# Kernel tuning notes

Hardware: AMD Instinct MI355X
Metric: run time of the kernel (lower is better)

## Reference

```python
import jax, jax.numpy as jnp
import numpy as np

N = 20000      # num_nodes / scatter_size
F = 128        # dataset_num_features
H = 8          # heads
HID = 64       # hidden_channels
REP = 512      # represent_features
NCLS = 133     # dataset_num_classes
E = 200000     # num edges (== num synapses)
PTS = 4        # points per synapse
P = E * PTS    # total synapse points

# Eval-mode semantics: dropout = identity; PyG MLP BatchNorm with fresh
# running stats (mean=0, var=1, affine=1/0) = identity. GATConv has no
# edge_dim, so edge_attr does not enter the math (kept as an input for parity).

def _glorot(key, shape):
    fan_in, fan_out = shape[0], shape[-1]
    if len(shape) == 3:  # attention vectors [H, C]: PyG treats as (1, H*C)
        fan_in, fan_out = 1, shape[-2] * shape[-1]
    lim = jnp.sqrt(6.0 / (fan_in + fan_out))
    return jax.random.uniform(key, shape, jnp.float32, -lim, lim)


def setup_inputs() -> dict:
    key = jax.random.key(0)
    ks = jax.random.split(key, 20)
    edge_index = jax.random.randint(ks[0], (2, E), 0, N, dtype=jnp.int32)
    edge_attr = jax.random.normal(ks[1], (E, 1), jnp.float32)
    synapse = jax.random.normal(ks[2], (P, 6), jnp.float32)
    # every synapse (edge) owns PTS points -> no empty segments for max-pool
    synapse_index = (jnp.arange(P, dtype=jnp.int32) // PTS)
    inp = {
        "edge_index": edge_index,
        "edge_attr": edge_attr,
        "synapse": synapse,
        "synapse_index": synapse_index,
        "scatter_size": N,
        # learned node embedding (nn.Parameter, xavier)
        "x_param": _glorot(ks[3], (N, F)),
        # GATConv 1: F -> H*HID
        "W1": _glorot(ks[4], (F, H * HID)),
        "att_src1": _glorot(ks[5], (1, H, HID))[0],
        "att_dst1": _glorot(ks[6], (1, H, HID))[0],
        "b1": jnp.zeros((H * HID,), jnp.float32),
        # GATConv 2: H*HID -> REP, heads=1, concat=False
        "W2": _glorot(ks[7], (H * HID, REP)),
        "att_src2": _glorot(ks[8], (1, 1, REP))[0],
        "att_dst2": _glorot(ks[9], (1, 1, REP))[0],
        "b2": jnp.zeros((REP,), jnp.float32),
        # synapse_encoder MLP([6, 256, 512])
        "We1": _glorot(ks[10], (6, 256)),
        "be1": jnp.zeros((256,), jnp.float32),
        "We2": _glorot(ks[11], (256, 512)),
        "be2": jnp.zeros((512,), jnp.float32),
        # classmodel MLP([1536, 512, 133])
        "Wc1": _glorot(ks[12], (1536, 512)),
        "bc1": jnp.zeros((512,), jnp.float32),
        "Wc2": _glorot(ks[13], (512, NCLS)),
        "bc2": jnp.zeros((NCLS,), jnp.float32),
    }
    return inp


def _gat_conv(x, src, dst, n, W, a_src, a_dst, b, heads, ch, concat):
    # x: [n, Fin]; src/dst already include self-loops (PyG default)
    xl = (x @ W).reshape(n, heads, ch)                 # [n, H, C]
    s = jnp.einsum('nhc,hc->nh', xl, a_src)            # alpha_src
    d = jnp.einsum('nhc,hc->nh', xl, a_dst)            # alpha_dst
    alpha = jax.nn.leaky_relu(s[src] + d[dst], negative_slope=0.2)  # [Ee, H]
    amax = jax.ops.segment_max(alpha, dst, num_segments=n)
    ex = jnp.exp(alpha - amax[dst])
    den = jax.ops.segment_sum(ex, dst, num_segments=n)
    a = ex / (den[dst] + 1e-16)                        # segment softmax
    out = jax.ops.segment_sum(xl[src] * a[:, :, None], dst, num_segments=n)
    out = out.reshape(n, heads * ch) if concat else out.mean(axis=1)
    return out + b


def _scatter_mean(vals, idx, n):
    s = jax.ops.segment_sum(vals, idx, num_segments=n)
    cnt = jax.ops.segment_sum(jnp.ones((vals.shape[0],), vals.dtype), idx, num_segments=n)
    return s / jnp.maximum(cnt, 1.0)[:, None]


def reference(edge_index, edge_attr, synapse, synapse_index, scatter_size,
              x_param, W1, att_src1, att_dst1, b1, W2, att_src2, att_dst2, b2,
              We1, be1, We2, be2, Wc1, bc1, Wc2, bc2):
    n = scatter_size
    loop = jnp.arange(n, dtype=edge_index.dtype)
    src = jnp.concatenate([edge_index[0], loop])   # GATConv adds self-loops
    dst = jnp.concatenate([edge_index[1], loop])

    x = jax.nn.elu(_gat_conv(x_param, src, dst, n, W1, att_src1, att_dst1, b1, H, HID, True))
    x = _gat_conv(x, src, dst, n, W2, att_src2, att_dst2, b2, 1, REP, False)   # [n, REP]

    # global_max_pool over synapse points -> one 6-vec per edge
    x_point = jax.ops.segment_max(synapse, synapse_index, num_segments=E)      # [E, 6]
    x_point = jax.nn.relu(x_point @ We1 + be1) @ We2 + be2                      # [E, 512]

    left = _scatter_mean(x_point, edge_index[0], n)
    right = _scatter_mean(x_point, edge_index[1], n)

    final = jnp.concatenate([x, left, right], axis=1)                           # [n, 1536]
    pred = jax.nn.relu(final @ Wc1 + bc1) @ Wc2 + bc2
    return pred
```

## Files before the change

kernel.cpp:

```cpp
#include <hip/hip_runtime.h>
#include <cstddef>

#define NN   20000
#define FEAT 128
#define NH   8
#define NE   200000
#define EE   220000

typedef _Float16 f16;
typedef _Float16 f16x2 __attribute__((ext_vector_type(2)));
typedef _Float16 f16x8 __attribute__((ext_vector_type(8)));
typedef float    f32x4 __attribute__((ext_vector_type(4)));

__device__ __forceinline__ float lrelu(float a) { return a > 0.f ? a : 0.2f * a; }

#define PB0 782
#define PB1 (PB0 + 782)
#define PB2 (PB1 + 10064)
#define PB3 (PB2 + 10)
#define PB4 (PB3 + 128)
#define PB5 (PB4 + 80)
__global__ __launch_bounds__(256) void preamble(
    const int* __restrict__ ei, const float* __restrict__ syn,
    const float* __restrict__ W1, const float* __restrict__ xparam,
    const float* __restrict__ W2, const float* __restrict__ We2,
    const float* __restrict__ Wc1, const float* __restrict__ Wc2,
    const float* __restrict__ b2, const float* __restrict__ be2,
    const float* __restrict__ as2, const float* __restrict__ ad2,
    int* __restrict__ dL, int* __restrict__ dR,
    float* __restrict__ xp, f16* __restrict__ W1t, f16* __restrict__ xph,
    f16* __restrict__ WzAt, f16* __restrict__ McatT, f16* __restrict__ Wc2t,
    float* __restrict__ vB, float* __restrict__ vL, float* __restrict__ vR,
    float* __restrict__ ws2, float* __restrict__ wd2)
{
  __shared__ float smem[2112];
  const int b = blockIdx.x, t = threadIdx.x;
  if (b < PB0) {
    int e = b * 256 + t;
    if (e >= NE) return;
    atomicAdd(&dL[ei[e]], 1);
    atomicAdd(&dR[ei[NE + e]], 1);
  } else if (b < PB1) {
    int e = (b - PB0) * 256 + t;
    if (e >= NE) return;
    const float* p = syn + (size_t)e * 24;
    float v[24];
#pragma unroll
    for (int i = 0; i < 6; i++) {
      float4 q = *(const float4*)(p + i * 4);
      v[i*4+0] = q.x; v[i*4+1] = q.y; v[i*4+2] = q.z; v[i*4+3] = q.w;
    }
#pragma unroll
    for (int dd = 0; dd < 6; dd++)
      xp[(size_t)e * 6 + dd] = fmaxf(fmaxf(v[dd], v[6 + dd]), fmaxf(v[12 + dd], v[18 + dd]));
  } else if (b < PB2) {
    int bb = b - PB1;
    if (bb < 64) {
      float (*tile)[33] = (float(*)[33])smem;
      const int n0 = (bb & 15) * 32, k0 = (bb >> 4) * 32;
      const int tx = t & 31, ty = t >> 5;
#pragma unroll
      for (int i = 0; i < 4; i++)
        tile[ty + i * 8][tx] = W1[(size_t)(k0 + ty + i * 8) * 512 + n0 + tx];
      __syncthreads();
#pragma unroll
      for (int i = 0; i < 4; i++)
        W1t[(size_t)(n0 + ty + i * 8) * 128 + k0 + tx] = (f16)tile[tx][ty + i * 8];
    } else {
      int idx = (bb - 64) * 256 + t;
      xph[idx] = (f16)xparam[idx];
    }
  } else if (b < PB3) {
    int g = (b - PB2) * 256 + t;
    int seg = g >> 9, j = g & 511;
    float a = 0.f;
    if (seg == 0) {
      for (int k = 0; k < 512; k++) a = fmaf(b2[k], Wc1[(size_t)k * 512 + j], a);
      vB[j] = a;
    } else if (seg == 1) {
      for (int k = 0; k < 512; k++) a = fmaf(be2[k], Wc1[(size_t)(512 + k) * 512 + j], a);
      vL[j] = a;
    } else if (seg == 2) {
      for (int k = 0; k < 512; k++) a = fmaf(be2[k], Wc1[(size_t)(1024 + k) * 512 + j], a);
      vR[j] = a;
    } else if (seg == 3) {
      for (int c = 0; c < 512; c++) a = fmaf(W2[(size_t)j * 512 + c], as2[c], a);
      ws2[j] = a;
    } else {
      for (int c = 0; c < 512; c++) a = fmaf(W2[(size_t)j * 512 + c], ad2[c], a);
      wd2[j] = a;
    }
  } else if (b < PB4) {
    float (*As)[68] = (float(*)[68])smem;
    float (*Bs)[64] = (float(*)[64])(smem + 16 * 68);
    const int bb = b - PB3;
    const float* A; const float* B; f16* dst; int dstOff, m0, n0;
    if (bb < 64)      { A = W2;  B = Wc1;  dst = WzAt;  dstOff = 0;
                        m0 = (bb >> 3) * 64; n0 = (bb & 7) * 64; }
    else if (bb < 96) { int i = bb - 64; A = We2; B = Wc1 + (size_t)512 * 512;
                        dst = McatT; dstOff = 0;
                        m0 = (i >> 3) * 64; n0 = (i & 7) * 64; }
    else              { int i = bb - 96; A = We2; B = Wc1 + (size_t)1024 * 512;
                        dst = McatT; dstOff = 256;
                        m0 = (i >> 3) * 64; n0 = (i & 7) * 64; }
    const int tx = t & 15, ty = t >> 4;
    float acc[4][4] = {{0.f}};
    float pa[4], pb[4];
#pragma unroll
    for (int i = 0; i < 4; i++) {
      int idx = t + i * 256;
      pa[i] = A[(size_t)(m0 + (idx >> 4)) * 512 + (idx & 15)];
      pb[i] = B[(size_t)(idx >> 6) * 512 + n0 + (idx & 63)];
    }
    for (int k0 = 0; k0 < 512; k0 += 16) {
#pragma unroll
      for (int i = 0; i < 4; i++) {
        int idx = t + i * 256;
        As[idx & 15][idx >> 4] = pa[i];
        Bs[idx >> 6][idx & 63] = pb[i];
      }
      __syncthreads();
      if (k0 + 16 < 512) {
        int kn = k0 + 16;
#pragma unroll
        for (int i = 0; i < 4; i++) {
          int idx = t + i * 256;
          pa[i] = A[(size_t)(m0 + (idx >> 4)) * 512 + kn + (idx & 15)];
          pb[i] = B[(size_t)(kn + (idx >> 6)) * 512 + n0 + (idx & 63)];
        }
      }
#pragma unroll
      for (int kk = 0; kk < 16; kk++) {
        float4 a4 = *(const float4*)&As[kk][ty * 4];
        float4 b4 = *(const float4*)&Bs[kk][tx * 4];
        float av[4] = {a4.x, a4.y, a4.z, a4.w};
        float bv[4] = {b4.x, b4.y, b4.z, b4.w};
#pragma unroll
        for (int i = 0; i < 4; i++)
#pragma unroll
          for (int j = 0; j < 4; j++) acc[i][j] = fmaf(av[i], bv[j], acc[i][j]);
      }
      __syncthreads();
    }
#pragma unroll
    for (int i = 0; i < 4; i++)
#pragma unroll
      for (int j = 0; j < 4; j++)
        dst[(size_t)(n0 + tx * 4 + j) * 512 + dstOff + m0 + ty * 4 + i] = (f16)acc[i][j];
  } else {
    float (*tile)[33] = (float(*)[33])smem;
    int i0 = b - PB4;
    const int n0 = (i0 % 5) * 32, k0 = (i0 / 5) * 32;
    const int tx = t & 31, ty = t >> 5;
#pragma unroll
    for (int i = 0; i < 4; i++) {
      int k = k0 + ty + i * 8, n = n0 + tx;
      tile[ty + i * 8][tx] = (n < 133) ? Wc2[(size_t)k * 133 + n] : 0.f;
    }
    __syncthreads();
#pragma unroll
    for (int i = 0; i < 4; i++) {
      int n = n0 + ty + i * 8, k = k0 + tx;
      if (n < 133) Wc2t[(size_t)n * 512 + k] = (f16)tile[tx][ty + i * 8];
    }
  }
}

__global__ __launch_bounds__(256) void fused1(
    const f16* __restrict__ xph, const f16* __restrict__ W1t, f16* __restrict__ xl1h,
    const float* __restrict__ xp, const float* __restrict__ We1,
    const float* __restrict__ be1,
    const int* __restrict__ oL, const int* __restrict__ eL,
    const int* __restrict__ oR, const int* __restrict__ eR,
    f16* __restrict__ hlrh)
{
  __shared__ __align__(16) f16 smem[7680];
  const int t = threadIdx.x;
  if (blockIdx.x < 1252) {
    f16 (*As)[40] = (f16(*)[40])smem;
    f16 (*Bs)[40] = (f16(*)[40])(smem + 64 * 40);
    const int wave = t >> 6, lane = t & 63;
    const int quad = lane >> 4, mrow = lane & 15;
    const int m0 = (blockIdx.x >> 2) * 64, n0 = (blockIdx.x & 3) * 128;
    f32x4 acc[4][2];
    f32x4 zero4 = {0.f, 0.f, 0.f, 0.f};
#pragma unroll
    for (int i = 0; i < 4; i++)
#pragma unroll
      for (int j = 0; j < 2; j++) acc[i][j] = zero4;
    const int ar = t >> 2, ac = (t & 3) * 8;
    for (int k0 = 0; k0 < FEAT; k0 += 32) {
      {
        int gm = m0 + ar;
        f16x8 v = {0, 0, 0, 0, 0, 0, 0, 0};
        if (gm < NN) v = *(const f16x8*)(xph + (size_t)gm * FEAT + k0 + ac);
        *(f16x8*)&As[ar][ac] = v;
      }
#pragma unroll
      for (int i = 0; i < 2; i++) {
        int idx = t + i * 256;
        int r = idx >> 2, c = (idx & 3) * 8;
        *(f16x8*)&Bs[r][c] = *(const f16x8*)(W1t + (size_t)(n0 + r) * FEAT + k0 + c);
      }
      __syncthreads();
      f16x8 af[4], bf[2];
#pragma unroll
      for (int mt = 0; mt < 4; mt++) af[mt] = *(const f16x8*)&As[mt * 16 + mrow][quad * 8];
#pragma unroll
      for (int nt = 0; nt < 2; nt++) bf[nt] = *(const f16x8*)&Bs[wave * 32 + nt * 16 + mrow][quad * 8];
#pragma unroll
      for (int mt = 0; mt < 4; mt++)
#pragma unroll
        for (int nt = 0; nt < 2; nt++)
          acc[mt][nt] = __builtin_amdgcn_mfma_f32_16x16x32_f16(af[mt], bf[nt], acc[mt][nt], 0, 0, 0);
      __syncthreads();
    }
#pragma unroll
    for (int mt = 0; mt < 4; mt++)
#pragma unroll
      for (int nt = 0; nt < 2; nt++) {
        int col = n0 + wave * 32 + nt * 16 + mrow;
#pragma unroll
        for (int reg = 0; reg < 4; reg++) {
          int row = m0 + mt * 16 + quad * 4 + reg;
          if (row < NN) xl1h[(size_t)row * 512 + col] = (f16)acc[mt][nt][reg];
        }
      }
  } else {
    int* lst_s  = (int*)smem;
    f16x2* xs2  = (f16x2*)(smem + 128);
    const int b = blockIdx.x - 1252;
    const int c = t;
    const int* off; const int* lst; int n;
    if (b < NN) { off = oL; lst = eL; n = b; } else { off = oR; lst = eR; n = b - NN; }
    f16x2 w[6], bb2, zero2;
#pragma unroll
    for (int j = 0; j < 6; j++) { f16 wv = (f16)We1[j * 256 + c]; w[j][0] = wv; w[j][1] = wv; }
    { f16 bv = (f16)be1[c]; bb2[0] = bv; bb2[1] = bv; }
    zero2[0] = (f16)0.f; zero2[1] = (f16)0.f;
    const int beg = off[n], end = off[n + 1], deg = end - beg;
    f16x2 acc2 = zero2;
    float accT = 0.f;
    for (int base = 0; base < deg; base += 32) {
      int m = min(32, deg - base);
      if (c < 32) lst_s[c] = (c < m) ? lst[beg + base + c] : 0;
      __syncthreads();
      if (c < 96) {
        int j = c / 6, cc = c - j * 6;
        int e0 = 2 * j, e1 = 2 * j + 1;
        float v0 = (e0 < m) ? xp[(size_t)lst_s[e0] * 6 + cc] : 0.f;
        float v1 = (e1 < m) ? xp[(size_t)lst_s[e1] * 6 + cc] : 0.f;
        f16x2 pr; pr[0] = (f16)v0; pr[1] = (f16)v1;
        xs2[j * 6 + cc] = pr;
      }
      __syncthreads();
      int mp = m >> 1;
      for (int k = 0; k < mp; k++) {
        f16x2 v = bb2;
#pragma unroll
        for (int j = 0; j < 6; j++) v = xs2[k * 6 + j] * w[j] + v;
        f16x2 r;
        r[0] = v[0] > (f16)0.f ? v[0] : (f16)0.f;
        r[1] = v[1] > (f16)0.f ? v[1] : (f16)0.f;
        acc2 = acc2 + r;
      }
      if (m & 1) {
        float v = (float)bb2[0];
#pragma unroll
        for (int j = 0; j < 6; j++) v = fmaf((float)xs2[mp * 6 + j][0], (float)w[j][0], v);
        accT += fmaxf(v, 0.f);
      }
    }
    float accf = (float)acc2[0] + (float)acc2[1] + accT;
    hlrh[(size_t)b * 256 + c] = (f16)(deg > 0 ? accf / (float)deg : 0.f);
  }
}

__global__ __launch_bounds__(256) void fused2(
    const f16* __restrict__ x1h, const f16* __restrict__ WzAt, f16* __restrict__ zh,
    const f16* __restrict__ hlrh, const f16* __restrict__ McatT,
    const int* __restrict__ degL, const int* __restrict__ degR,
    const float* __restrict__ bc1, const float* __restrict__ vB,
    const float* __restrict__ vL, const float* __restrict__ vR, f16* __restrict__ Ph)
{
  __shared__ __align__(16) f16 smem[7680];
  const int t = threadIdx.x;
  f16 (*As)[40] = (f16(*)[40])smem;
  f16 (*Bs)[40] = (f16(*)[40])(smem + 64 * 40);
  const bool isZ = blockIdx.x < 1252;
  const int bb = isZ ? blockIdx.x : blockIdx.x - 1252;
  const int wave = t >> 6, lane = t & 63;
  const int quad = lane >> 4, mrow = lane & 15;
  const int m0 = (bb >> 2) * 64, n0 = (bb & 3) * 128;
  f32x4 acc[4][2];
  f32x4 zero4 = {0.f, 0.f, 0.f, 0.f};
#pragma unroll
  for (int i = 0; i < 4; i++)
#pragma unroll
    for (int j = 0; j < 2; j++) acc[i][j] = zero4;
  const int ar = t >> 2, ac = (t & 3) * 8;
  const f16* Bt = isZ ? WzAt : McatT;
  for (int k0 = 0; k0 < 512; k0 += 32) {
    {
      int gm = m0 + ar;
      f16x8 v = {0, 0, 0, 0, 0, 0, 0, 0};
      if (gm < NN) {
        if (isZ) v = *(const f16x8*)(x1h + (size_t)gm * 512 + k0 + ac);
        else {
          size_t row = (k0 >> 8) ? (size_t)(NN + gm) : (size_t)gm;
          v = *(const f16x8*)(hlrh + row * 256 + (k0 & 255) + ac);
        }
      }
      *(f16x8*)&As[ar][ac] = v;
    }
#pragma unroll
    for (int i = 0; i < 2; i++) {
      int idx = t + i * 256;
      int r = idx >> 2, c = (idx & 3) * 8;
      *(f16x8*)&Bs[r][c] = *(const f16x8*)(Bt + (size_t)(n0 + r) * 512 + k0 + c);
    }
    __syncthreads();
    f16x8 af[4], bf[2];
#pragma unroll
    for (int mt = 0; mt < 4; mt++) af[mt] = *(const f16x8*)&As[mt * 16 + mrow][quad * 8];
#pragma unroll
    for (int nt = 0; nt < 2; nt++) bf[nt] = *(const f16x8*)&Bs[wave * 32 + nt * 16 + mrow][quad * 8];
#pragma unroll
    for (int mt = 0; mt < 4; mt++)
#pragma unroll
      for (int nt = 0; nt < 2; nt++)
        acc[mt][nt] = __builtin_amdgcn_mfma_f32_16x16x32_f16(af[mt], bf[nt], acc[mt][nt], 0, 0, 0);
    __syncthreads();
  }
  if (isZ) {
#pragma unroll
    for (int mt = 0; mt < 4; mt++)
#pragma unroll
      for (int nt = 0; nt < 2; nt++) {
        int col = n0 + wave * 32 + nt * 16 + mrow;
#pragma unroll
        for (int reg = 0; reg < 4; reg++) {
          int row = m0 + mt * 16 + quad * 4 + reg;
          if (row < NN) zh[(size_t)row * 512 + col] = (f16)acc[mt][nt][reg];
        }
      }
  } else {
#pragma unroll
    for (int mt = 0; mt < 4; mt++)
#pragma unroll
      for (int nt = 0; nt < 2; nt++) {
        int col = n0 + wave * 32 + nt * 16 + mrow;
        float bb2 = bc1[col] + vB[col];
        float vl = vL[col], vr = vR[col];
#pragma unroll
        for (int reg = 0; reg < 4; reg++) {
          int row = m0 + mt * 16 + quad * 4 + reg;
          if (row >= NN) continue;
          float v = acc[mt][nt][reg] + bb2;
          if (degL[row] > 0) v += vl;
          if (degR[row] > 0) v += vr;
          Ph[(size_t)row * 512 + col] = (f16)v;
        }
      }
  }
}

__global__ __launch_bounds__(256) void mfma_out(
    const f16* __restrict__ A, const f16* __restrict__ Bt,
    const float* __restrict__ bias, float* __restrict__ C, int M)
{
  __shared__ __align__(16) f16 As[64][40];
  __shared__ __align__(16) f16 Bs[128][40];
  const int t = threadIdx.x;
  const int wave = t >> 6, lane = t & 63;
  const int quad = lane >> 4, mrow = lane & 15;
  const int m0 = blockIdx.y * 64, n0 = blockIdx.x * 128;
  f32x4 acc[4][2];
  f32x4 zero4 = {0.f, 0.f, 0.f, 0.f};
#pragma unroll
  for (int i = 0; i < 4; i++)
#pragma unroll
    for (int j = 0; j < 2; j++) acc[i][j] = zero4;
  const int ar = t >> 2, ac = (t & 3) * 8;
  for (int k0 = 0; k0 < 512; k0 += 32) {
    {
      int gm = m0 + ar;
      f16x8 v = {0, 0, 0, 0, 0, 0, 0, 0};
      if (gm < M) v = *(const f16x8*)(A + (size_t)gm * 512 + k0 + ac);
      *(f16x8*)&As[ar][ac] = v;
    }
#pragma unroll
    for (int i = 0; i < 2; i++) {
      int idx = t + i * 256;
      int r = idx >> 2, c = (idx & 3) * 8;
      f16x8 v = {0, 0, 0, 0, 0, 0, 0, 0};
      if (n0 + r < 133) v = *(const f16x8*)(Bt + (size_t)(n0 + r) * 512 + k0 + c);
      *(f16x8*)&Bs[r][c] = v;
    }
    __syncthreads();
    f16x8 af[4], bf[2];
#pragma unroll
    for (int mt = 0; mt < 4; mt++) af[mt] = *(const f16x8*)&As[mt * 16 + mrow][quad * 8];
#pragma unroll
    for (int nt = 0; nt < 2; nt++) bf[nt] = *(const f16x8*)&Bs[wave * 32 + nt * 16 + mrow][quad * 8];
#pragma unroll
    for (int mt = 0; mt < 4; mt++)
#pragma unroll
      for (int nt = 0; nt < 2; nt++)
        acc[mt][nt] = __builtin_amdgcn_mfma_f32_16x16x32_f16(af[mt], bf[nt], acc[mt][nt], 0, 0, 0);
    __syncthreads();
  }
#pragma unroll
  for (int mt = 0; mt < 4; mt++)
#pragma unroll
    for (int nt = 0; nt < 2; nt++) {
      int col = n0 + wave * 32 + nt * 16 + mrow;
      if (col >= 133) continue;
      float bb = bias[col];
#pragma unroll
      for (int reg = 0; reg < 4; reg++) {
        int row = m0 + mt * 16 + quad * 4 + reg;
        if (row < M) C[(size_t)row * 133 + col] = acc[mt][nt][reg] + bb;
      }
    }
}

__global__ __launch_bounds__(1024) void scan_csr(
    const int* __restrict__ dL, const int* __restrict__ dR,
    int* __restrict__ oL, int* __restrict__ oR, int* __restrict__ oA)
{
  const int b = blockIdx.x;
  const int* deg = b == 0 ? dL : dR;
  __shared__ int part[1024];
  const int t = threadIdx.x;
  const int chunk = 20;
  int base = t * chunk;
  int sum = 0;
  for (int i = 0; i < chunk; i++) { int idx = base + i; if (idx < NN) sum += deg[idx]; }
  part[t] = sum;
  __syncthreads();
  for (int o = 1; o < 1024; o <<= 1) {
    int v = (t >= o) ? part[t - o] : 0;
    __syncthreads();
    part[t] += v;
    __syncthreads();
  }
  int run = part[t] - sum;
  if (b == 0) {
    for (int i = 0; i < chunk; i++) {
      int idx = base + i;
      if (idx < NN) { oL[idx] = run; run += deg[idx]; }
    }
    if (t == 0) oL[NN] = part[1023];
  } else {
    for (int i = 0; i < chunk; i++) {
      int idx = base + i;
      if (idx < NN) { oR[idx] = run; oA[idx] = run + idx; run += deg[idx]; }
    }
    if (t == 0) { oR[NN] = part[1023]; oA[NN] = part[1023] + NN; }
  }
}

__global__ __launch_bounds__(256) void fill_csr(
    const int* __restrict__ ei,
    const int* __restrict__ oL, const int* __restrict__ oR, const int* __restrict__ oA,
    int* __restrict__ cL, int* __restrict__ cR,
    int* __restrict__ eL, int* __restrict__ eR, int* __restrict__ snA)
{
  int e = blockIdx.x * 256 + threadIdx.x;
  if (e >= EE) return;
  if (e < NE) {
    int s = ei[e], d = ei[NE + e];
    int p = atomicAdd(&cL[s], 1); eL[oL[s] + p] = e;
    p = atomicAdd(&cR[d], 1);
    eR[oR[d] + p] = e;
    snA[oA[d] + 1 + p] = s;
  } else {
    int n = e - NE;
    snA[oA[n]] = n;
  }
}

__global__ __launch_bounds__(256) void attn_dots1(
    const f16* __restrict__ xlh, const float* __restrict__ asrc,
    const float* __restrict__ adst, float* __restrict__ s, float* __restrict__ d)
{
  int gid = blockIdx.x * 256 + threadIdx.x;
  if (gid >= NN * NH) return;
  int n = gid >> 3, h = gid & 7;
  const f16x2* row = (const f16x2*)(xlh + (size_t)n * 512 + h * 64);
  const float* a1 = asrc + h * 64;
  const float* a2 = adst + h * 64;
  float ss = 0.f, dd = 0.f;
#pragma unroll 8
  for (int j = 0; j < 32; j++) {
    f16x2 p = row[j];
    float v0 = (float)p[0], v1 = (float)p[1];
    ss += v0 * a1[2 * j] + v1 * a1[2 * j + 1];
    dd += v0 * a2[2 * j] + v1 * a2[2 * j + 1];
  }
  s[gid] = ss; d[gid] = dd;
}

__global__ __launch_bounds__(256) void gat_gather1(
    const int* __restrict__ snA, const int* __restrict__ offA,
    const float* __restrict__ s1, const float* __restrict__ d1,
    const f16* __restrict__ xlh, const float* __restrict__ b1,
    const float* __restrict__ ws2, const float* __restrict__ wd2,
    f16* __restrict__ x1h, float* __restrict__ s2, float* __restrict__ d2)
{
  __shared__ int sns[32];
  __shared__ float wls[256];
  __shared__ float red[256], redD[256];
  const int n = blockIdx.x, t = threadIdx.x;
  const int hw = t & 7;
  const int slot = t >> 3;
  const int hf = t >> 5;
  const int beg = offA[n], end = offA[n + 1];
  const int deg = end - beg;
  const float dnw = d1[n * 8 + hw];
  float a0 = 0.f, a1v = 0.f, denp = 0.f;
  for (int base = 0; base < deg; base += 32) {
    int m = min(32, deg - base);
    if (t < 32) sns[t] = (t < m) ? snA[beg + base + t] : 0;
    __syncthreads();
    {
      float w = 0.f;
      if (slot < m) w = __expf(lrelu(s1[sns[slot] * 8 + hw] + dnw));
      wls[t] = w;
      denp += w;
    }
    __syncthreads();
    int m8 = (m + 7) & ~7;
    for (int k = 0; k < m8; k += 8) {
      int ss[8]; float ww[8]; f16x2 pp[8];
#pragma unroll
      for (int u = 0; u < 8; u++) { ss[u] = sns[k + u]; ww[u] = wls[(k + u) * 8 + hf]; }
#pragma unroll
      for (int u = 0; u < 8; u++) pp[u] = *(const f16x2*)(xlh + (size_t)ss[u] * 512 + 2 * t);
#pragma unroll
      for (int u = 0; u < 8; u++) {
        a0  = fmaf(ww[u], (float)pp[u][0], a0);
        a1v = fmaf(ww[u], (float)pp[u][1], a1v);
      }
    }
    __syncthreads();
  }
  red[t] = denp;
  __syncthreads();
  for (int off = 128; off >= 8; off >>= 1) {
    if (t < off) red[t] += red[t + off];
    __syncthreads();
  }
  float rh = 1.f / (red[hf] + 1e-16f);
  __syncthreads();
  float v0 = a0 * rh + b1[2 * t], v1 = a1v * rh + b1[2 * t + 1];
  v0 = v0 > 0.f ? v0 : (__expf(v0) - 1.f);
  v1 = v1 > 0.f ? v1 : (__expf(v1) - 1.f);
  f16x2 o; o[0] = (f16)v0; o[1] = (f16)v1;
  *(f16x2*)(x1h + (size_t)n * 512 + 2 * t) = o;
  red[t]  = v0 * ws2[2 * t] + v1 * ws2[2 * t + 1];
  redD[t] = v0 * wd2[2 * t] + v1 * wd2[2 * t + 1];
  __syncthreads();
  for (int off = 128; off > 0; off >>= 1) {
    if (t < off) { red[t] += red[t + off]; redD[t] += redD[t + off]; }
    __syncthreads();
  }
  if (t == 0) { s2[n] = red[0]; d2[n] = redD[0]; }
}

__global__ __launch_bounds__(256) void gat_gather2(
    const int* __restrict__ snA, const int* __restrict__ offA,
    const float* __restrict__ s2, const float* __restrict__ d2,
    const f16* __restrict__ zh, const f16* __restrict__ Ph,
    f16* __restrict__ h2h)
{
  __shared__ int sns[32];
  __shared__ float wls[32];
  __shared__ float den_sh;
  const int n = blockIdx.x, t = threadIdx.x;
  const int beg = offA[n], end = offA[n + 1];
  const int deg = end - beg;
  const float dn = d2[n];
  float a0 = 0.f, a1v = 0.f, denp = 0.f;
  for (int base = 0; base < deg; base += 32) {
    int m = min(32, deg - base);
    if (t < 32) {
      int sn = (t < m) ? snA[beg + base + t] : 0;
      float w = (t < m) ? __expf(lrelu(s2[sn] + dn)) : 0.f;
      sns[t] = sn;
      wls[t] = w;
      denp += w;
    }
    __syncthreads();
    int m8 = (m + 7) & ~7;
    for (int k = 0; k < m8; k += 8) {
      int ss[8]; float ww[8]; f16x2 pp[8];
#pragma unroll
      for (int u = 0; u < 8; u++) { ss[u] = sns[k + u]; ww[u] = wls[k + u]; }
#pragma unroll
      for (int u = 0; u < 8; u++) pp[u] = *(const f16x2*)(zh + (size_t)ss[u] * 512 + 2 * t);
#pragma unroll
      for (int u = 0; u < 8; u++) {
        a0  = fmaf(ww[u], (float)pp[u][0], a0);
        a1v = fmaf(ww[u], (float)pp[u][1], a1v);
      }
    }
    __syncthreads();
  }
  if (t < 64) {
    denp += __shfl_xor(denp, 16);
    denp += __shfl_xor(denp, 8);
    denp += __shfl_xor(denp, 4);
    denp += __shfl_xor(denp, 2);
    denp += __shfl_xor(denp, 1);
    if (t == 0) den_sh = denp;
  }
  __syncthreads();
  float rn = 1.f / (den_sh + 1e-16f);
  f16x2 pv = *(const f16x2*)(Ph + (size_t)n * 512 + 2 * t);
  float v0 = fmaxf(a0  * rn + (float)pv[0], 0.f);
  float v1 = fmaxf(a1v * rn + (float)pv[1], 0.f);
  f16x2 o; o[0] = (f16)v0; o[1] = (f16)v1;
  *(f16x2*)(h2h + (size_t)n * 512 + 2 * t) = o;
}

extern "C" void kernel_launch(void* const* d_in, const int* in_sizes, int n_in,
                              void* d_out, int out_size, void* d_ws, size_t ws_size,
                              hipStream_t stream) {
  const int*   edge_index = (const int*)d_in[0];
  const float* synapse    = (const float*)d_in[2];
  const float* x_param = (const float*)d_in[5];
  const float* W1      = (const float*)d_in[6];
  const float* as1     = (const float*)d_in[7];
  const float* ad1     = (const float*)d_in[8];
  const float* b1      = (const float*)d_in[9];
  const float* W2      = (const float*)d_in[10];
  const float* as2     = (const float*)d_in[11];
  const float* ad2     = (const float*)d_in[12];
  const float* b2      = (const float*)d_in[13];
  const float* We1     = (const float*)d_in[14];
  const float* be1     = (const float*)d_in[15];
  const float* We2     = (const float*)d_in[16];
  const float* be2     = (const float*)d_in[17];
  const float* Wc1     = (const float*)d_in[18];
  const float* bc1     = (const float*)d_in[19];
  const float* Wc2     = (const float*)d_in[20];
  const float* bc2     = (const float*)d_in[21];
  float* out_p = (float*)d_out;

  char* p = (char*)d_ws;
  float* xp    = (float*)p; p += (size_t)NE * 6 * 4;
  float* s1    = (float*)p; p += (size_t)NN * 8 * 4;
  float* d1    = (float*)p; p += (size_t)NN * 8 * 4;
  float* s2    = (float*)p; p += (size_t)NN * 4;
  float* d2    = (float*)p; p += (size_t)NN * 4;
  float* vB    = (float*)p; p += 512 * 4;
  float* vL    = (float*)p; p += 512 * 4;
  float* vR    = (float*)p; p += 512 * 4;
  float* ws2   = (float*)p; p += 512 * 4;
  float* wd2   = (float*)p; p += 512 * 4;
  f16* xph     = (f16*)p; p += (size_t)NN * FEAT * 2;
  f16* xl1h    = (f16*)p; p += (size_t)NN * 512 * 2;
  f16* x1h     = (f16*)p; p += (size_t)NN * 512 * 2;
  f16* zh      = (f16*)p; p += (size_t)NN * 512 * 2;
  f16* h2h     = (f16*)p; p += (size_t)NN * 512 * 2;
  f16* Phb     = (f16*)p; p += (size_t)NN * 512 * 2;
  f16* hlrh    = (f16*)p; p += (size_t)2 * NN * 256 * 2;
  f16* W1t     = (f16*)p; p += (size_t)512 * FEAT * 2;
  f16* WzAt    = (f16*)p; p += (size_t)512 * 512 * 2;
  f16* McatT   = (f16*)p; p += (size_t)512 * 512 * 2;
  f16* Wc2t    = (f16*)p; p += (size_t)133 * 512 * 2;
  int* degL    = (int*)p;
  int* degR    = degL + NN;
  int* curL    = degR + NN;
  int* curR    = curL + NN;
  int* offL    = curR + NN;
  int* offR    = offL + NN + 1;
  int* offA    = offR + NN + 1;
  int* edgeL   = offA + NN + 1;
  int* edgeR   = edgeL + NE;
  int* snA     = edgeR + NE;

  hipMemsetAsync(degL, 0, (size_t)4 * NN * sizeof(int), stream);

  preamble<<<PB5, 256, 0, stream>>>(
      edge_index, synapse, W1, x_param, W2, We2, Wc1, Wc2, b2, be2, as2, ad2,
      degL, degR, xp, W1t, xph, WzAt, McatT, Wc2t, vB, vL, vR, ws2, wd2);
  scan_csr<<<2, 1024, 0, stream>>>(degL, degR, offL, offR, offA);
  fill_csr<<<(EE + 255) / 256, 256, 0, stream>>>(edge_index, offL, offR, offA,
                                                 curL, curR, edgeL, edgeR, snA);
  fused1<<<1252 + 2 * NN, 256, 0, stream>>>(xph, W1t, xl1h, xp, We1, be1,
                                            offL, edgeL, offR, edgeR, hlrh);
  attn_dots1<<<(NN * NH + 255) / 256, 256, 0, stream>>>(xl1h, as1, ad1, s1, d1);
  gat_gather1<<<NN, 256, 0, stream>>>(snA, offA, s1, d1, xl1h, b1, ws2, wd2,
                                      x1h, s2, d2);
  fused2<<<2504, 256, 0, stream>>>(x1h, WzAt, zh, hlrh, McatT,
                                   degL, degR, bc1, vB, vL, vR, Phb);
  gat_gather2<<<NN, 256, 0, stream>>>(snA, offA, s2, d2, zh, Phb, h2h);
  mfma_out<<<dim3(2, 313), 256, 0, stream>>>(h2h, Wc2t, bc2, out_p, NN);
}
```

Before: 489.4 us.

## Fuse attention dots into GEMM epilogue and rebalance weight prep across kernels

The layer-1 attention dot products are now computed in the fused1 GEMM epilogue from an LDS tile, which removes the separate attn_dots1 kernel and its re-read of xl1h. Each edge-pooling block now handles 16 nodes instead of one, cutting the block count from 40000 to 2500. The weight-product GEMMs and the Wc2 transpose move out of the preamble into a new mid_kernel, where they run as extra blocks beside the gather1 work, shortening the critical path through the preamble. The costs are heavier per-block serialization in the pooling path and an extra LDS tile write in the GEMM epilogue.

```diff
diff --git a/kernel.cpp b/kernel.cpp
--- a/kernel.cpp
+++ b/kernel.cpp
@@ -14,34 +14,30 @@
 
 __device__ __forceinline__ float lrelu(float a) { return a > 0.f ? a : 0.2f * a; }
 
-#define PB0 782
-#define PB1 (PB0 + 782)
-#define PB2 (PB1 + 10064)
-#define PB3 (PB2 + 10)
-#define PB4 (PB3 + 128)
-#define PB5 (PB4 + 80)
-__global__ __launch_bounds__(256) void preamble(
+#define PA0 782
+#define PA1 (PA0 + 782)
+#define PA2 (PA1 + 10064)
+#define PA3 (PA2 + 10)
+__global__ __launch_bounds__(256) void preambleA(
     const int* __restrict__ ei, const float* __restrict__ syn,
     const float* __restrict__ W1, const float* __restrict__ xparam,
-    const float* __restrict__ W2, const float* __restrict__ We2,
-    const float* __restrict__ Wc1, const float* __restrict__ Wc2,
+    const float* __restrict__ W2, const float* __restrict__ Wc1,
     const float* __restrict__ b2, const float* __restrict__ be2,
     const float* __restrict__ as2, const float* __restrict__ ad2,
     int* __restrict__ dL, int* __restrict__ dR,
     float* __restrict__ xp, f16* __restrict__ W1t, f16* __restrict__ xph,
-    f16* __restrict__ WzAt, f16* __restrict__ McatT, f16* __restrict__ Wc2t,
     float* __restrict__ vB, float* __restrict__ vL, float* __restrict__ vR,
     float* __restrict__ ws2, float* __restrict__ wd2)
 {
-  __shared__ float smem[2112];
+  __shared__ float smem[1056];
   const int b = blockIdx.x, t = threadIdx.x;
-  if (b < PB0) {
+  if (b < PA0) {
     int e = b * 256 + t;
     if (e >= NE) return;
     atomicAdd(&dL[ei[e]], 1);
     atomicAdd(&dR[ei[NE + e]], 1);
-  } else if (b < PB1) {
-    int e = (b - PB0) * 256 + t;
+  } else if (b < PA1) {
+    int e = (b - PA0) * 256 + t;
     if (e >= NE) return;
     const float* p = syn + (size_t)e * 24;
     float v[24];
@@ -53,8 +49,8 @@
 #pragma unroll
     for (int dd = 0; dd < 6; dd++)
       xp[(size_t)e * 6 + dd] = fmaxf(fmaxf(v[dd], v[6 + dd]), fmaxf(v[12 + dd], v[18 + dd]));
-  } else if (b < PB2) {
-    int bb = b - PB1;
+  } else if (b < PA2) {
+    int bb = b - PA1;
     if (bb < 64) {
       float (*tile)[33] = (float(*)[33])smem;
       const int n0 = (bb & 15) * 32, k0 = (bb >> 4) * 32;
@@ -70,8 +66,8 @@
       int idx = (bb - 64) * 256 + t;
       xph[idx] = (f16)xparam[idx];
     }
-  } else if (b < PB3) {
-    int g = (b - PB2) * 256 + t;
+  } else {
+    int g = (b - PA2) * 256 + t;
     int seg = g >> 9, j = g & 511;
     float a = 0.f;
     if (seg == 0) {
@@ -90,10 +86,226 @@
       for (int c = 0; c < 512; c++) a = fmaf(W2[(size_t)j * 512 + c], ad2[c], a);
       wd2[j] = a;
     }
-  } else if (b < PB4) {
+  }
+}
+
+__global__ __launch_bounds__(256) void fused1(
+    const f16* __restrict__ xph, const f16* __restrict__ W1t, f16* __restrict__ xl1h,
+    const float* __restrict__ as1, const float* __restrict__ ad1,
+    float* __restrict__ s1, float* __restrict__ d1,
+    const float* __restrict__ xp, const float* __restrict__ We1,
+    const float* __restrict__ be1,
+    const int* __restrict__ oL, const int* __restrict__ eL,
+    const int* __restrict__ oR, const int* __restrict__ eR,
+    f16* __restrict__ hlrh)
+{
+  __shared__ __align__(16) f16 smem[8320];
+  const int t = threadIdx.x;
+  if (blockIdx.x < 1252) {
+    f16 (*As)[40] = (f16(*)[40])smem;
+    f16 (*Bs)[40] = (f16(*)[40])(smem + 64 * 40);
+    const int wave = t >> 6, lane = t & 63;
+    const int quad = lane >> 4, mrow = lane & 15;
+    const int m0 = (blockIdx.x >> 2) * 64, n0 = (blockIdx.x & 3) * 128;
+    f32x4 acc[4][2];
+    f32x4 zero4 = {0.f, 0.f, 0.f, 0.f};
+#pragma unroll
+    for (int i = 0; i < 4; i++)
+#pragma unroll
+      for (int j = 0; j < 2; j++) acc[i][j] = zero4;
+    const int ar = t >> 2, ac = (t & 3) * 8;
+    for (int k0 = 0; k0 < FEAT; k0 += 32) {
+      {
+        int gm = m0 + ar;
+        f16x8 v = {0, 0, 0, 0, 0, 0, 0, 0};
+        if (gm < NN) v = *(const f16x8*)(xph + (size_t)gm * FEAT + k0 + ac);
+        *(f16x8*)&As[ar][ac] = v;
+      }
+#pragma unroll
+      for (int i = 0; i < 2; i++) {
+        int idx = t + i * 256;
+        int r = idx >> 2, c = (idx & 3) * 8;
+        *(f16x8*)&Bs[r][c] = *(const f16x8*)(W1t + (size_t)(n0 + r) * FEAT + k0 + c);
+      }
+      __syncthreads();
+      f16x8 af[4], bf[2];
+#pragma unroll
+      for (int mt = 0; mt < 4; mt++) af[mt] = *(const f16x8*)&As[mt * 16 + mrow][quad * 8];
+#pragma unroll
+      for (int nt = 0; nt < 2; nt++) bf[nt] = *(const f16x8*)&Bs[wave * 32 + nt * 16 + mrow][quad * 8];
+#pragma unroll
+      for (int mt = 0; mt < 4; mt++)
+#pragma unroll
+        for (int nt = 0; nt < 2; nt++)
+          acc[mt][nt] = __builtin_amdgcn_mfma_f32_16x16x32_f16(af[mt], bf[nt], acc[mt][nt], 0, 0, 0);
+      __syncthreads();
+    }
+    f16 (*tile)[130] = (f16(*)[130])smem;
+#pragma unroll
+    for (int mt = 0; mt < 4; mt++)
+#pragma unroll
+      for (int nt = 0; nt < 2; nt++) {
+        int cl = wave * 32 + nt * 16 + mrow;
+        int col = n0 + cl;
+#pragma unroll
+        for (int reg = 0; reg < 4; reg++) {
+          int rl = mt * 16 + quad * 4 + reg;
+          int row = m0 + rl;
+          f16 cv = (f16)acc[mt][nt][reg];
+          tile[rl][cl] = cv;
+          if (row < NN) xl1h[(size_t)row * 512 + col] = cv;
+        }
+      }
+    __syncthreads();
+    {
+      int pair = t >> 1, half = t & 1;
+      int rl = pair & 63, hl = pair >> 6;
+      int h = (n0 >> 6) + hl;
+      const float* a1 = as1 + h * 64 + half * 32;
+      const float* a2 = ad1 + h * 64 + half * 32;
+      const f16* trow = &tile[rl][hl * 64 + half * 32];
+      float ssum = 0.f, dsum = 0.f;
+#pragma unroll 8
+      for (int j = 0; j < 32; j++) {
+        float v = (float)trow[j];
+        ssum += v * a1[j];
+        dsum += v * a2[j];
+      }
+      ssum += __shfl_down(ssum, 1);
+      dsum += __shfl_down(dsum, 1);
+      int row = m0 + rl;
+      if (!half && row < NN) { s1[row * 8 + h] = ssum; d1[row * 8 + h] = dsum; }
+    }
+  } else {
+    int* lst_s  = (int*)smem;
+    f16x2* xs2  = (f16x2*)(smem + 128);
+    const int c = t;
+    f16x2 w[6], bb2, zero2;
+#pragma unroll
+    for (int j = 0; j < 6; j++) { f16 wv = (f16)We1[j * 256 + c]; w[j][0] = wv; w[j][1] = wv; }
+    { f16 bv = (f16)be1[c]; bb2[0] = bv; bb2[1] = bv; }
+    zero2[0] = (f16)0.f; zero2[1] = (f16)0.f;
+    const int b0 = (blockIdx.x - 1252) * 16;
+    for (int q = 0; q < 16; q++) {
+      const int b = b0 + q;
+      const int* off; const int* lst; int n;
+      if (b < NN) { off = oL; lst = eL; n = b; } else { off = oR; lst = eR; n = b - NN; }
+      const int beg = off[n], end = off[n + 1], deg = end - beg;
+      f16x2 acc2 = zero2;
+      float accT = 0.f;
+      for (int base = 0; base < deg; base += 32) {
+        int m = min(32, deg - base);
+        if (c < 32) lst_s[c] = (c < m) ? lst[beg + base + c] : 0;
+        __syncthreads();
+        if (c < 96) {
+          int j = c / 6, cc = c - j * 6;
+          int e0 = 2 * j, e1 = 2 * j + 1;
+          float v0 = (e0 < m) ? xp[(size_t)lst_s[e0] * 6 + cc] : 0.f;
+          float v1 = (e1 < m) ? xp[(size_t)lst_s[e1] * 6 + cc] : 0.f;
+          f16x2 pr; pr[0] = (f16)v0; pr[1] = (f16)v1;
+          xs2[j * 6 + cc] = pr;
+        }
+        __syncthreads();
+        int mp = m >> 1;
+        for (int k = 0; k < mp; k++) {
+          f16x2 v = bb2;
+#pragma unroll
+          for (int j = 0; j < 6; j++) v = xs2[k * 6 + j] * w[j] + v;
+          f16x2 r;
+          r[0] = v[0] > (f16)0.f ? v[0] : (f16)0.f;
+          r[1] = v[1] > (f16)0.f ? v[1] : (f16)0.f;
+          acc2 = acc2 + r;
+        }
+        if (m & 1) {
+          float v = (float)bb2[0];
+#pragma unroll
+          for (int j = 0; j < 6; j++) v = fmaf((float)xs2[mp * 6 + j][0], (float)w[j][0], v);
+          accT += fmaxf(v, 0.f);
+        }
+        __syncthreads();
+      }
+      float accf = (float)acc2[0] + (float)acc2[1] + accT;
+      hlrh[(size_t)b * 256 + c] = (f16)(deg > 0 ? accf / (float)deg : 0.f);
+    }
+  }
+}
+
+__global__ __launch_bounds__(256) void mid_kernel(
+    const int* __restrict__ snA, const int* __restrict__ offA,
+    const float* __restrict__ s1, const float* __restrict__ d1,
+    const f16* __restrict__ xlh, const float* __restrict__ b1,
+    const float* __restrict__ ws2, const float* __restrict__ wd2,
+    f16* __restrict__ x1h, float* __restrict__ s2, float* __restrict__ d2,
+    const float* __restrict__ W2, const float* __restrict__ We2,
+    const float* __restrict__ Wc1, f16* __restrict__ WzAt, f16* __restrict__ McatT,
+    const float* __restrict__ Wc2, f16* __restrict__ Wc2t)
+{
+  __shared__ float smem[2112];
+  const int t = threadIdx.x;
+  if (blockIdx.x < NN) {
+    int* sns   = (int*)smem;
+    float* wls = smem + 32;
+    float* red = smem + 288;
+    float* redD= smem + 544;
+    const int n = blockIdx.x;
+    const int hw = t & 7;
+    const int slot = t >> 3;
+    const int hf = t >> 5;
+    const int beg = offA[n], end = offA[n + 1];
+    const int deg = end - beg;
+    const float dnw = d1[n * 8 + hw];
+    float a0 = 0.f, a1v = 0.f, denp = 0.f;
+    for (int base = 0; base < deg; base += 32) {
+      int m = min(32, deg - base);
+      if (t < 32) sns[t] = (t < m) ? snA[beg + base + t] : 0;
+      __syncthreads();
+      {
+        float w = 0.f;
+        if (slot < m) w = __expf(lrelu(s1[sns[slot] * 8 + hw] + dnw));
+        wls[t] = w;
+        denp += w;
+      }
+      __syncthreads();
+      int m8 = (m + 7) & ~7;
+      for (int k = 0; k < m8; k += 8) {
+        int ss[8]; float ww[8]; f16x2 pp[8];
+#pragma unroll
+        for (int u = 0; u < 8; u++) { ss[u] = sns[k + u]; ww[u] = wls[(k + u) * 8 + hf]; }
+#pragma unroll
+        for (int u = 0; u < 8; u++) pp[u] = *(const f16x2*)(xlh + (size_t)ss[u] * 512 + 2 * t);
+#pragma unroll
+        for (int u = 0; u < 8; u++) {
+          a0  = fmaf(ww[u], (float)pp[u][0], a0);
+          a1v = fmaf(ww[u], (float)pp[u][1], a1v);
+        }
+      }
+      __syncthreads();
+    }
+    red[t] = denp;
+    __syncthreads();
+    for (int off = 128; off >= 8; off >>= 1) {
+      if (t < off) red[t] += red[t + off];
+      __syncthreads();
+    }
+    float rh = 1.f / (red[hf] + 1e-16f);
+    __syncthreads();
+    float v0 = a0 * rh + b1[2 * t], v1 = a1v * rh + b1[2 * t + 1];
+    v0 = v0 > 0.f ? v0 : (__expf(v0) - 1.f);
+    v1 = v1 > 0.f ? v1 : (__expf(v1) - 1.f);
+    f16x2 o; o[0] = (f16)v0; o[1] = (f16)v1;
+    *(f16x2*)(x1h + (size_t)n * 512 + 2 * t) = o;
+    red[t]  = v0 * ws2[2 * t] + v1 * ws2[2 * t + 1];
+    redD[t] = v0 * wd2[2 * t] + v1 * wd2[2 * t + 1];
+    __syncthreads();
+    for (int off = 128; off > 0; off >>= 1) {
+      if (t < off) { red[t] += red[t + off]; redD[t] += redD[t + off]; }
+      __syncthreads();
+    }
+    if (t == 0) { s2[n] = red[0]; d2[n] = redD[0]; }
+  } else if (blockIdx.x < NN + 128) {
     float (*As)[68] = (float(*)[68])smem;
     float (*Bs)[64] = (float(*)[64])(smem + 16 * 68);
-    const int bb = b - PB3;
+    const int bb = blockIdx.x - NN;
     const float* A; const float* B; f16* dst; int dstOff, m0, n0;
     if (bb < 64)      { A = W2;  B = Wc1;  dst = WzAt;  dstOff = 0;
                         m0 = (bb >> 3) * 64; n0 = (bb & 7) * 64; }
@@ -149,7 +361,7 @@
         dst[(size_t)(n0 + tx * 4 + j) * 512 + dstOff + m0 + ty * 4 + i] = (f16)acc[i][j];
   } else {
     float (*tile)[33] = (float(*)[33])smem;
-    int i0 = b - PB4;
+    int i0 = blockIdx.x - NN - 128;
     const int n0 = (i0 % 5) * 32, k0 = (i0 / 5) * 32;
     const int tx = t & 31, ty = t >> 5;
 #pragma unroll
@@ -163,116 +375,6 @@
       int n = n0 + ty + i * 8, k = k0 + tx;
       if (n < 133) Wc2t[(size_t)n * 512 + k] = (f16)tile[tx][ty + i * 8];
     }
-  }
-}
-
-__global__ __launch_bounds__(256) void fused1(
-    const f16* __restrict__ xph, const f16* __restrict__ W1t, f16* __restrict__ xl1h,
-    const float* __restrict__ xp, const float* __restrict__ We1,
-    const float* __restrict__ be1,
-    const int* __restrict__ oL, const int* __restrict__ eL,
-    const int* __restrict__ oR, const int* __restrict__ eR,
-    f16* __restrict__ hlrh)
-{
-  __shared__ __align__(16) f16 smem[7680];
-  const int t = threadIdx.x;
-  if (blockIdx.x < 1252) {
-    f16 (*As)[40] = (f16(*)[40])smem;
-    f16 (*Bs)[40] = (f16(*)[40])(smem + 64 * 40);
-    const int wave = t >> 6, lane = t & 63;
-    const int quad = lane >> 4, mrow = lane & 15;
-    const int m0 = (blockIdx.x >> 2) * 64, n0 = (blockIdx.x & 3) * 128;
-    f32x4 acc[4][2];
-    f32x4 zero4 = {0.f, 0.f, 0.f, 0.f};
-#pragma unroll
-    for (int i = 0; i < 4; i++)
-#pragma unroll
-      for (int j = 0; j < 2; j++) acc[i][j] = zero4;
-    const int ar = t >> 2, ac = (t & 3) * 8;
-    for (int k0 = 0; k0 < FEAT; k0 += 32) {
-      {
-        int gm = m0 + ar;
-        f16x8 v = {0, 0, 0, 0, 0, 0, 0, 0};
-        if (gm < NN) v = *(const f16x8*)(xph + (size_t)gm * FEAT + k0 + ac);
-        *(f16x8*)&As[ar][ac] = v;
-      }
-#pragma unroll
-      for (int i = 0; i < 2; i++) {
-        int idx = t + i * 256;
-        int r = idx >> 2, c = (idx & 3) * 8;
-        *(f16x8*)&Bs[r][c] = *(const f16x8*)(W1t + (size_t)(n0 + r) * FEAT + k0 + c);
-      }
-      __syncthreads();
-      f16x8 af[4], bf[2];
-#pragma unroll
-      for (int mt = 0; mt < 4; mt++) af[mt] = *(const f16x8*)&As[mt * 16 + mrow][quad * 8];
-#pragma unroll
-      for (int nt = 0; nt < 2; nt++) bf[nt] = *(const f16x8*)&Bs[wave * 32 + nt * 16 + mrow][quad * 8];
-#pragma unroll
-      for (int mt = 0; mt < 4; mt++)
-#pragma unroll
-        for (int nt = 0; nt < 2; nt++)
-          acc[mt][nt] = __builtin_amdgcn_mfma_f32_16x16x32_f16(af[mt], bf[nt], acc[mt][nt], 0, 0, 0);
-      __syncthreads();
-    }
-#pragma unroll
-    for (int mt = 0; mt < 4; mt++)
-#pragma unroll
-      for (int nt = 0; nt < 2; nt++) {
-        int col = n0 + wave * 32 + nt * 16 + mrow;
-#pragma unroll
-        for (int reg = 0; reg < 4; reg++) {
-          int row = m0 + mt * 16 + quad * 4 + reg;
-          if (row < NN) xl1h[(size_t)row * 512 + col] = (f16)acc[mt][nt][reg];
-        }
-      }
-  } else {
-    int* lst_s  = (int*)smem;
-    f16x2* xs2  = (f16x2*)(smem + 128);
-    const int b = blockIdx.x - 1252;
-    const int c = t;
-    const int* off; const int* lst; int n;
-    if (b < NN) { off = oL; lst = eL; n = b; } else { off = oR; lst = eR; n = b - NN; }
-    f16x2 w[6], bb2, zero2;
-#pragma unroll
-    for (int j = 0; j < 6; j++) { f16 wv = (f16)We1[j * 256 + c]; w[j][0] = wv; w[j][1] = wv; }
-    { f16 bv = (f16)be1[c]; bb2[0] = bv; bb2[1] = bv; }
-    zero2[0] = (f16)0.f; zero2[1] = (f16)0.f;
-    const int beg = off[n], end = off[n + 1], deg = end - beg;
-    f16x2 acc2 = zero2;
-    float accT = 0.f;
-    for (int base = 0; base < deg; base += 32) {
-      int m = min(32, deg - base);
-      if (c < 32) lst_s[c] = (c < m) ? lst[beg + base + c] : 0;
-      __syncthreads();
-      if (c < 96) {
-        int j = c / 6, cc = c - j * 6;
-        int e0 = 2 * j, e1 = 2 * j + 1;
-        float v0 = (e0 < m) ? xp[(size_t)lst_s[e0] * 6 + cc] : 0.f;
-        float v1 = (e1 < m) ? xp[(size_t)lst_s[e1] * 6 + cc] : 0.f;
-        f16x2 pr; pr[0] = (f16)v0; pr[1] = (f16)v1;
-        xs2[j * 6 + cc] = pr;
-      }
-      __syncthreads();
-      int mp = m >> 1;
-      for (int k = 0; k < mp; k++) {
-        f16x2 v = bb2;
-#pragma unroll
-        for (int j = 0; j < 6; j++) v = xs2[k * 6 + j] * w[j] + v;
-        f16x2 r;
-        r[0] = v[0] > (f16)0.f ? v[0] : (f16)0.f;
-        r[1] = v[1] > (f16)0.f ? v[1] : (f16)0.f;
-        acc2 = acc2 + r;
-      }
-      if (m & 1) {
-        float v = (float)bb2[0];
-#pragma unroll
-        for (int j = 0; j < 6; j++) v = fmaf((float)xs2[mp * 6 + j][0], (float)w[j][0], v);
-        accT += fmaxf(v, 0.f);
-      }
-    }
-    float accf = (float)acc2[0] + (float)acc2[1] + accT;
-    hlrh[(size_t)b * 256 + c] = (f16)(deg > 0 ? accf / (float)deg : 0.f);
   }
 }
 
@@ -479,94 +581,6 @@
     int n = e - NE;
     snA[oA[n]] = n;
   }
-}
-
-__global__ __launch_bounds__(256) void attn_dots1(
-    const f16* __restrict__ xlh, const float* __restrict__ asrc,
-    const float* __restrict__ adst, float* __restrict__ s, float* __restrict__ d)
-{
-  int gid = blockIdx.x * 256 + threadIdx.x;
-  if (gid >= NN * NH) return;
-  int n = gid >> 3, h = gid & 7;
-  const f16x2* row = (const f16x2*)(xlh + (size_t)n * 512 + h * 64);
-  const float* a1 = asrc + h * 64;
-  const float* a2 = adst + h * 64;
-  float ss = 0.f, dd = 0.f;
-#pragma unroll 8
-  for (int j = 0; j < 32; j++) {
-    f16x2 p = row[j];
-    float v0 = (float)p[0], v1 = (float)p[1];
-    ss += v0 * a1[2 * j] + v1 * a1[2 * j + 1];
-    dd += v0 * a2[2 * j] + v1 * a2[2 * j + 1];
-  }
-  s[gid] = ss; d[gid] = dd;
-}
-
-__global__ __launch_bounds__(256) void gat_gather1(
-    const int* __restrict__ snA, const int* __restrict__ offA,
-    const float* __restrict__ s1, const float* __restrict__ d1,
-    const f16* __restrict__ xlh, const float* __restrict__ b1,
-    const float* __restrict__ ws2, const float* __restrict__ wd2,
-    f16* __restrict__ x1h, float* __restrict__ s2, float* __restrict__ d2)
-{
-  __shared__ int sns[32];
-  __shared__ float wls[256];
-  __shared__ float red[256], redD[256];
-  const int n = blockIdx.x, t = threadIdx.x;
-  const int hw = t & 7;
-  const int slot = t >> 3;
-  const int hf = t >> 5;
-  const int beg = offA[n], end = offA[n + 1];
-  const int deg = end - beg;
-  const float dnw = d1[n * 8 + hw];
-  float a0 = 0.f, a1v = 0.f, denp = 0.f;
-  for (int base = 0; base < deg; base += 32) {
-    int m = min(32, deg - base);
-    if (t < 32) sns[t] = (t < m) ? snA[beg + base + t] : 0;
-    __syncthreads();
-    {
-      float w = 0.f;
-      if (slot < m) w = __expf(lrelu(s1[sns[slot] * 8 + hw] + dnw));
-      wls[t] = w;
-      denp += w;
-    }
-    __syncthreads();
-    int m8 = (m + 7) & ~7;
-    for (int k = 0; k < m8; k += 8) {
-      int ss[8]; float ww[8]; f16x2 pp[8];
-#pragma unroll
-      for (int u = 0; u < 8; u++) { ss[u] = sns[k + u]; ww[u] = wls[(k + u) * 8 + hf]; }
-#pragma unroll
-      for (int u = 0; u < 8; u++) pp[u] = *(const f16x2*)(xlh + (size_t)ss[u] * 512 + 2 * t);
-#pragma unroll
-      for (int u = 0; u < 8; u++) {
-        a0  = fmaf(ww[u], (float)pp[u][0], a0);
-        a1v = fmaf(ww[u], (float)pp[u][1], a1v);
-      }
-    }
-    __syncthreads();
-  }
-  red[t] = denp;
-  __syncthreads();
-  for (int off = 128; off >= 8; off >>= 1) {
-    if (t < off) red[t] += red[t + off];
-    __syncthreads();
-  }
-  float rh = 1.f / (red[hf] + 1e-16f);
-  __syncthreads();
-  float v0 = a0 * rh + b1[2 * t], v1 = a1v * rh + b1[2 * t + 1];
-  v0 = v0 > 0.f ? v0 : (__expf(v0) - 1.f);
-  v1 = v1 > 0.f ? v1 : (__expf(v1) - 1.f);
-  f16x2 o; o[0] = (f16)v0; o[1] = (f16)v1;
-  *(f16x2*)(x1h + (size_t)n * 512 + 2 * t) = o;
-  red[t]  = v0 * ws2[2 * t] + v1 * ws2[2 * t + 1];
-  redD[t] = v0 * wd2[2 * t] + v1 * wd2[2 * t + 1];
-  __syncthreads();
-  for (int off = 128; off > 0; off >>= 1) {
-    if (t < off) { red[t] += red[t + off]; redD[t] += redD[t + off]; }
-    __syncthreads();
-  }
-  if (t == 0) { s2[n] = red[0]; d2[n] = redD[0]; }
 }
 
 __global__ __launch_bounds__(256) void gat_gather2(
@@ -684,17 +698,17 @@
 
   hipMemsetAsync(degL, 0, (size_t)4 * NN * sizeof(int), stream);
 
-  preamble<<<PB5, 256, 0, stream>>>(
-      edge_index, synapse, W1, x_param, W2, We2, Wc1, Wc2, b2, be2, as2, ad2,
-      degL, degR, xp, W1t, xph, WzAt, McatT, Wc2t, vB, vL, vR, ws2, wd2);
+  preambleA<<<PA3, 256, 0, stream>>>(
+      edge_index, synapse, W1, x_param, W2, Wc1, b2, be2, as2, ad2,
+      degL, degR, xp, W1t, xph, vB, vL, vR, ws2, wd2);
   scan_csr<<<2, 1024, 0, stream>>>(degL, degR, offL, offR, offA);
   fill_csr<<<(EE + 255) / 256, 256, 0, stream>>>(edge_index, offL, offR, offA,
                                                  curL, curR, edgeL, edgeR, snA);
-  fused1<<<1252 + 2 * NN, 256, 0, stream>>>(xph, W1t, xl1h, xp, We1, be1,
-                                            offL, edgeL, offR, edgeR, hlrh);
-  attn_dots1<<<(NN * NH + 255) / 256, 256, 0, stream>>>(xl1h, as1, ad1, s1, d1);
-  gat_gather1<<<NN, 256, 0, stream>>>(snA, offA, s1, d1, xl1h, b1, ws2, wd2,
-                                      x1h, s2, d2);
+  fused1<<<1252 + 2500, 256, 0, stream>>>(xph, W1t, xl1h, as1, ad1, s1, d1,
+                                          xp, We1, be1, offL, edgeL, offR, edgeR, hlrh);
+  mid_kernel<<<NN + 208, 256, 0, stream>>>(snA, offA, s1, d1, xl1h, b1, ws2, wd2,
+                                           x1h, s2, d2, W2, We2, Wc1, WzAt, McatT,
+                                           Wc2, Wc2t);
   fused2<<<2504, 256, 0, stream>>>(x1h, WzAt, zh, hlrh, McatT,
                                    degL, degR, bc1, vB, vL, vR, Phb);
   gat_gather2<<<NN, 256, 0, stream>>>(snA, offA, s2, d2, zh, Phb, h2h);
```

Result: slower. 499.5 us (+2.1%).
